# Optimization experiments

Hardware: AMD Instinct MI355X
Metric: run time of the kernel (lower is better)

## Reference

```python
import jax, jax.numpy as jnp
import numpy as np


def setup_inputs() -> dict:
    key = jax.random.key(0)
    kx, ky = jax.random.split(key)
    x = jax.random.normal(kx, (176, 64, 56, 56), dtype=jnp.float32)
    y = jax.random.normal(ky, (176, 128, 28, 28), dtype=jnp.float32)
    return {"x": x, "y": y}


def reference(x, y):
    # Faithful to: unfold(x, k=s, stride=s) -> view(B,C1,s*s,H2,W2) ->
    # cat each patch-position slice with y -> fold back to (H1,W1).
    # For non-overlapping patches, fold(unfold(x)) == x, and y is placed at
    # every within-block offset, i.e. nearest-neighbor upsampled by s.
    B, C1, H1, W1 = x.shape
    _, C2, H2, W2 = y.shape
    s = H1 // H2  # = 2
    # out[:, C1:, h, w] = y[:, :, h//s, w//s]
    y_up = jnp.repeat(jnp.repeat(y, s, axis=2), s, axis=3)  # (B, C2, H1, W1)
    return jnp.concatenate([x, y_up], axis=1)  # (B, C1+C2, H1, W1)
```

## Files before the change

kernel.cpp:

```cpp
#include <hip/hip_runtime.h>


#define NB   176
#define C1   64
#define C2   128
#define HH   56
#define WW   56
#define H2   28
#define W2   28
#define CT   (C1 + C2)
#define VPR  (WW / 4)
#define NROWS (NB * CT * HH)
#define NVEC  (NROWS * VPR)

__global__ __launch_bounds__(256) void upcat_kernel(
    const float* __restrict__ x,
    const float* __restrict__ y,
    float* __restrict__ out)
{
    int i = blockIdx.x * blockDim.x + threadIdx.x;
    if (i >= NVEC) return;

    int r  = i / VPR;
    int j  = i - r * VPR;
    int w0 = j * 4;

    int h  = r % HH;
    int bc = r / HH;
    int c  = bc % CT;
    int b  = bc / CT;

    float4 v;
    if (c < C1) {
        const float4* px = (const float4*)(x + ((b * C1 + c) * HH + h) * WW + w0);
        v = *px;
    } else {
        int c2 = c - C1;
        const float2* py = (const float2*)(y + ((b * C2 + c2) * H2 + (h >> 1)) * W2 + (w0 >> 1));
        float2 u = *py;
        v = make_float4(u.x, u.x, u.y, u.y);
    }

    float4* po = (float4*)(out + r * WW + w0);
    *po = v;
}

extern "C" void kernel_launch(void* const* d_in, const int* in_sizes, int n_in,
                              void* d_out, int out_size, void* d_ws, size_t ws_size,
                              hipStream_t stream) {
    const float* x = (const float*)d_in[0];
    const float* y = (const float*)d_in[1];
    float* out = (float*)d_out;

    int nblocks = (NVEC + 255) / 256;
    upcat_kernel<<<nblocks, 256, 0, stream>>>(x, y, out);
}
```

Before: 529.7 us.

## Index by source element, write two output rows per y load, use nontemporal ops

Threads are now mapped over input vectors instead of output vectors. Each y float2 is loaded once and written to both upsampled output rows, which removes the duplicate y reads that came from neighbouring output rows. All loads and stores use nontemporal builtins to avoid polluting the cache on this streaming copy. The grid size is hardcoded with no bounds check, so it depends on the exact shape dividing evenly.

```diff
diff --git a/kernel.cpp b/kernel.cpp
--- a/kernel.cpp
+++ b/kernel.cpp
@@ -1,17 +1,11 @@
 #include <hip/hip_runtime.h>
 
 
-#define NB   176
-#define C1   64
-#define C2   128
-#define HH   56
-#define WW   56
-#define H2   28
-#define W2   28
-#define CT   (C1 + C2)
-#define VPR  (WW / 4)
-#define NROWS (NB * CT * HH)
-#define NVEC  (NROWS * VPR)
+typedef float vf4 __attribute__((ext_vector_type(4)));
+typedef float vf2 __attribute__((ext_vector_type(2)));
+
+#define NXV 8830976
+#define NYV 8830976
 
 __global__ __launch_bounds__(256) void upcat_kernel(
     const float* __restrict__ x,
@@ -19,30 +13,33 @@
     float* __restrict__ out)
 {
     int i = blockIdx.x * blockDim.x + threadIdx.x;
-    if (i >= NVEC) return;
 
-    int r  = i / VPR;
-    int j  = i - r * VPR;
-    int w0 = j * 4;
+    if (i < NXV) {
+        int r  = i / 14;
+        int j  = i - r * 14;
+        int b  = r / 3584;
+        int cr = r - b * 3584;
 
-    int h  = r % HH;
-    int bc = r / HH;
-    int c  = bc % CT;
-    int b  = bc / CT;
+        vf4 v = __builtin_nontemporal_load((const vf4*)(x + r * 56 + 4 * j));
+        __builtin_nontemporal_store(v, (vf4*)(out + b * 602112 + cr * 56 + 4 * j));
+    } else {
+        int k   = i - NXV;
+        int ry  = k / 14;
+        int j   = k - ry * 14;
 
-    float4 v;
-    if (c < C1) {
-        const float4* px = (const float4*)(x + ((b * C1 + c) * HH + h) * WW + w0);
-        v = *px;
-    } else {
-        int c2 = c - C1;
-        const float2* py = (const float2*)(y + ((b * C2 + c2) * H2 + (h >> 1)) * W2 + (w0 >> 1));
-        float2 u = *py;
-        v = make_float4(u.x, u.x, u.y, u.y);
+        vf2 u = __builtin_nontemporal_load((const vf2*)(y + ry * 28 + 2 * j));
+
+        int b   = ry / 3584;
+        int cr2 = ry - b * 3584;
+        int c2  = cr2 / 28;
+        int h2  = cr2 - c2 * 28;
+
+        vf4 v;
+        v.x = u.x; v.y = u.x; v.z = u.y; v.w = u.y;
+        int orow = (b * 192 + 64 + c2) * 56 + 2 * h2;
+        __builtin_nontemporal_store(v, (vf4*)(out + orow * 56 + 4 * j));
+        __builtin_nontemporal_store(v, (vf4*)(out + (orow + 1) * 56 + 4 * j));
     }
-
-    float4* po = (float4*)(out + r * WW + w0);
-    *po = v;
 }
 
 extern "C" void kernel_launch(void* const* d_in, const int* in_sizes, int n_in,
@@ -52,6 +49,5 @@
     const float* y = (const float*)d_in[1];
     float* out = (float*)d_out;
 
-    int nblocks = (NVEC + 255) / 256;
-    upcat_kernel<<<nblocks, 256, 0, stream>>>(x, y, out);
+    upcat_kernel<<<(NXV + NYV) / 256, 256, 0, stream>>>(x, y, out);
 }
```

After: 587.7 us. 1.11x slower.
